# Kernel optimization log

Hardware: AMD Instinct MI355X
Metric: run time of the kernel (lower is better)

The kernel has to match this reference:

```python
import jax, jax.numpy as jnp
import numpy as np

B, L, H = 32, 512, 1024
H2 = H // 2          # split half = 512
D_ATTN = 64
EPS = 1e-5


def setup_inputs() -> dict:
    key = jax.random.key(0)
    ks = jax.random.split(key, 6)
    x = jax.random.normal(ks[0], (B, L, H), dtype=jnp.float32)
    # LayerNorm params (default torch init: weight=1, bias=0)
    ln_gamma = jnp.ones((H2,), jnp.float32)
    ln_beta = jnp.zeros((H2,), jnp.float32)
    # Toeplitz params (module inits w_vector=0, bias=1; use small random w for nontrivial math)
    w_vector = jax.random.normal(ks[1], (2 * L - 1,), jnp.float32) * 0.02
    t_bias = jnp.ones((L,), jnp.float32)
    # TinyAttention: kqv Linear(H2 -> 3*d_attn), proj Linear(d_attn -> H2)
    kqv_w = jax.random.normal(ks[2], (H2, 3 * D_ATTN), jnp.float32) * 0.02
    kqv_b = jnp.zeros((3 * D_ATTN,), jnp.float32)
    proj_w = jax.random.normal(ks[3], (D_ATTN, H2), jnp.float32) * 0.02
    proj_b = jnp.zeros((H2,), jnp.float32)
    return {"x": x, "ln_gamma": ln_gamma, "ln_beta": ln_beta,
            "w_vector": w_vector, "t_bias": t_bias,
            "kqv_w": kqv_w, "kqv_b": kqv_b, "proj_w": proj_w, "proj_b": proj_b}


def _toeplitz(w_vector):
    # Faithful replication of get_toeplitz(): pad, tile, trim, reshape, crop.
    r = w_vector.shape[0] // 2            # = L - 1
    t = jnp.pad(w_vector, (0, L))         # length 3L - 1
    t = jnp.tile(t, L)[:-L]               # length L * (3L - 2)
    t = t.reshape(L, 3 * L - 2)
    return t[:, r:-r]                      # [L, L]


def _tiny_attention(v, kqv_w, kqv_b, proj_w, proj_b):
    kqv = v @ kqv_w + kqv_b                        # [B, L, 3*d_attn]
    k, q, val = jnp.split(kqv, 3, axis=-1)         # chunk order: key, query, value
    scale = 1.0 / jnp.sqrt(jnp.float32(q.shape[-1]))
    scores = jnp.einsum('bqd,bkd->bqk', q, k) * scale
    soft = jax.nn.softmax(scores, axis=-1)
    head = jnp.einsum('bqk,bkd->bqd', soft, val)   # [B, L, d_attn]
    return head @ proj_w + proj_b                  # [B, L, H2]


def reference(x, ln_gamma, ln_beta, w_vector, t_bias, kqv_w, kqv_b, proj_w, proj_b):
    u, v = jnp.split(x, 2, axis=-1)                # each [B, L, H2]
    head = _tiny_attention(v, kqv_w, kqv_b, proj_w, proj_b)
    # LayerNorm over last dim
    mu = jnp.mean(v, axis=-1, keepdims=True)
    var = jnp.mean(jnp.square(v - mu), axis=-1, keepdims=True)
    vn = (v - mu) * jax.lax.rsqrt(var + EPS) * ln_gamma + ln_beta
    # spatial (Toeplitz) mixing: permute -> [B, H2, L], matmul [L, L], bias
    w_t = _toeplitz(w_vector)
    vm = jnp.einsum('blc,lm->bmc', vn, w_t.T).transpose(0, 2, 1)  # keep faithful: vp @ w_t
    vm = jnp.einsum('bcl,lm->bcm', vn.transpose(0, 2, 1), w_t) + t_bias
    v_out = vm.transpose(0, 2, 1) + head           # [B, L, H2]
    return u * v_out
```

## Files before the change

kernel.cpp:

```cpp
#include <hip/hip_runtime.h>
#include <math.h>

#define NB 32
#define LL 512
#define HH 1024
#define H2 512
#define DA 64

typedef unsigned int u32;
typedef unsigned short u16;
typedef __bf16 bf16x8 __attribute__((ext_vector_type(8)));
typedef float f32x4 __attribute__((ext_vector_type(4)));

__device__ __forceinline__ u16 f2bu(float f) {
    u32 u = __builtin_bit_cast(u32, f);
    u = (u + 0x7fff + ((u >> 16) & 1)) >> 16;
    return (u16)u;
}

__device__ __forceinline__ float b2f(u16 u) {
    u32 v = (u32)u << 16;
    return __builtin_bit_cast(float, v);
}

__device__ __forceinline__ void async_cp16(const void* g, void* l) {
    __builtin_amdgcn_global_load_lds(
        (const __attribute__((address_space(1))) u32*)g,
        (__attribute__((address_space(3))) u32*)l, 16, 0, 0);
}

__global__ void prep_kernel(const float* __restrict__ wv,
                            const float* __restrict__ kqvw,
                            const float* __restrict__ projw,
                            u16* __restrict__ wt, u16* __restrict__ kqvwT,
                            u16* __restrict__ projwT) {
    int e = blockIdx.x * 256 + threadIdx.x;
    if (e < 262144) {
        int m = e >> 9, l = e & 511;
        wt[e] = f2bu(wv[511 + m - l]);
    } else if (e < 262144 + 98304) {
        int i = e - 262144;
        int n = i >> 9, k = i & 511;
        kqvwT[i] = f2bu(kqvw[(size_t)k * 192 + n]);
    } else {
        int i = e - 360448;
        int c = i >> 6, d = i & 63;
        projwT[i] = f2bu(projw[(size_t)d * 512 + c]);
    }
}

__global__ __launch_bounds__(256, 2)
void front_kernel(const float* __restrict__ x,
                  const float* __restrict__ gamma, const float* __restrict__ beta,
                  const u16* __restrict__ kqvwT, const float* __restrict__ kqvb,
                  u16* __restrict__ vnT,
                  u16* __restrict__ qb, u16* __restrict__ kb, u16* __restrict__ vT) {
    __shared__ u16 As[32 * 72];
    __shared__ u16 Bs[192 * 64];
    __shared__ u16 T[512 * 34];
    __shared__ float MUs[32], RSs[32];
    int blk = blockIdx.x, t = threadIdx.x;
    int b = blk >> 4, l0 = (blk & 15) * 32;
    int lane = t & 63, wid = t >> 6;
    int l15 = lane & 15, q16 = lane >> 4, q8 = q16 * 8;

#pragma unroll
    for (int s = 0; s < 6; ++s) {
        int ci = t + s * 256;
        int grow = ci >> 3, gcol = ((ci & 7) ^ (grow & 7)) << 3;
        async_cp16(kqvwT + (size_t)grow * 512 + gcol, Bs + ci * 8);
    }

    int r = t >> 3, q = t & 7;
    const float* xr = x + ((size_t)(b * LL + l0 + r)) * HH + H2;
    float s1 = 0.0f, s2 = 0.0f;
#pragma unroll
    for (int i = 0; i < 16; ++i) {
        float4 v = *(const float4*)(xr + q * 64 + i * 4);
        s1 += v.x + v.y + v.z + v.w;
        s2 += v.x * v.x + v.y * v.y + v.z * v.z + v.w * v.w;
        int c = q * 64 + i * 4;
        T[(c + 0) * 34 + r] = f2bu(v.x);
        T[(c + 1) * 34 + r] = f2bu(v.y);
        T[(c + 2) * 34 + r] = f2bu(v.z);
        T[(c + 3) * 34 + r] = f2bu(v.w);
    }
    s1 += __shfl_xor(s1, 1); s2 += __shfl_xor(s2, 1);
    s1 += __shfl_xor(s1, 2); s2 += __shfl_xor(s2, 2);
    s1 += __shfl_xor(s1, 4); s2 += __shfl_xor(s2, 4);
    float mu = s1 * (1.0f / H2);
    float rstd = rsqrtf(s2 * (1.0f / H2) - mu * mu + 1e-5f);
    if ((t & 7) == 0) { MUs[r] = mu; RSs[r] = rstd; }
    __syncthreads();

    {
        int cc = t >> 2, seg = t & 3;
        float m0 = MUs[seg * 8 + 0], r0s = RSs[seg * 8 + 0];
        float m1 = MUs[seg * 8 + 1], r1s = RSs[seg * 8 + 1];
        float m2 = MUs[seg * 8 + 2], r2s = RSs[seg * 8 + 2];
        float m3 = MUs[seg * 8 + 3], r3s = RSs[seg * 8 + 3];
        float m4 = MUs[seg * 8 + 4], r4s = RSs[seg * 8 + 4];
        float m5 = MUs[seg * 8 + 5], r5s = RSs[seg * 8 + 5];
        float m6 = MUs[seg * 8 + 6], r6s = RSs[seg * 8 + 6];
        float m7 = MUs[seg * 8 + 7], r7s = RSs[seg * 8 + 7];
#pragma unroll
        for (int pass = 0; pass < 8; ++pass) {
            int c = pass * 64 + cc;
            float ga = gamma[c], be = beta[c];
            const u16* Tp = T + c * 34 + seg * 8;
            ushort4 t0 = ((const ushort4*)Tp)[0];
            ushort4 t1 = ((const ushort4*)Tp)[1];
            ushort4 o0, o1;
            o0.x = f2bu((b2f(t0.x) - m0) * r0s * ga + be);
            o0.y = f2bu((b2f(t0.y) - m1) * r1s * ga + be);
            o0.z = f2bu((b2f(t0.z) - m2) * r2s * ga + be);
            o0.w = f2bu((b2f(t0.w) - m3) * r3s * ga + be);
            o1.x = f2bu((b2f(t1.x) - m4) * r4s * ga + be);
            o1.y = f2bu((b2f(t1.y) - m5) * r5s * ga + be);
            o1.z = f2bu((b2f(t1.z) - m6) * r6s * ga + be);
            o1.w = f2bu((b2f(t1.w) - m7) * r7s * ga + be);
            u16* dst = vnT + ((size_t)(b * H2 + c)) * LL + l0 + seg * 8;
            ((ushort4*)dst)[0] = o0;
            ((ushort4*)dst)[1] = o1;
        }
    }

    int wm = (wid & 1) * 16, wn = (wid >> 1) * 96;
    f32x4 acc[6] = {};
    for (int k0 = 0; k0 < 512; k0 += 64) {
        if (k0 > 0) {
#pragma unroll
            for (int s = 0; s < 6; ++s) {
                int ci = t + s * 256;
                int grow = ci >> 3, gcol = ((ci & 7) ^ (grow & 7)) << 3;
                async_cp16(kqvwT + (size_t)grow * 512 + k0 + gcol, Bs + ci * 8);
            }
        }
#pragma unroll
        for (int s = 0; s < 2; ++s) {
            int ci = t + s * 256;
            int row = ci >> 4, c4 = (ci & 15) * 4;
            float4 v = *(const float4*)(x + (size_t)(b * LL + l0 + row) * HH + H2 + k0 + c4);
            ushort4 p;
            p.x = f2bu(v.x); p.y = f2bu(v.y); p.z = f2bu(v.z); p.w = f2bu(v.w);
            *(ushort4*)(As + row * 72 + c4) = p;
        }
        __syncthreads();
#pragma unroll
        for (int kk = 0; kk < 2; ++kk) {
            int j0 = kk * 4 + q16;
            bf16x8 a = *(const bf16x8*)(As + (wm + l15) * 72 + kk * 32 + q8);
#pragma unroll
            for (int j = 0; j < 6; ++j) {
                int n = wn + j * 16 + l15;
                bf16x8 bb = *(const bf16x8*)(Bs + (n * 8 + (j0 ^ (n & 7))) * 8);
                acc[j] = __builtin_amdgcn_mfma_f32_16x16x32_bf16(a, bb, acc[j], 0, 0, 0);
            }
        }
        __syncthreads();
    }
    u16* Ts = As;
    int rq = q16 * 4;
#pragma unroll
    for (int rr = 0; rr < 4; ++rr) {
        int mloc = wm + rq + rr;
        size_t mg = (size_t)(b * LL + l0 + mloc);
#pragma unroll
        for (int j = 0; j < 6; ++j) {
            int n = wn + j * 16 + l15;
            u16 hv = f2bu(acc[j][rr] + kqvb[n]);
            if (n < 64)       kb[mg * 64 + n] = hv;
            else if (n < 128) qb[mg * 64 + (n - 64)] = hv;
            else              Ts[(n - 128) * 36 + mloc] = hv;
        }
    }
    __syncthreads();
    int d = t >> 2, lo2 = (t & 3) * 8;
    u16* dst = vT + ((size_t)(b * 64 + d)) * 512 + l0 + lo2;
    const u16* src = Ts + d * 36 + lo2;
    ((ushort4*)dst)[0] = ((const ushort4*)src)[0];
    ((ushort4*)dst)[1] = ((const ushort4*)src)[1];
}

#define VLD 136
__global__ __launch_bounds__(256, 4)
void attn_kernel(const u16* __restrict__ qb, const u16* __restrict__ kb,
                 const u16* __restrict__ vT, u16* __restrict__ head) {
    __shared__ u16 Ps[4 * 16 * VLD];
    __shared__ float Osh[4][16 * 65];
    __shared__ float Msh[4][16], Lsh[4][16];
    int b = blockIdx.y, q0 = blockIdx.x * 16;
    int t = threadIdx.x, lane = t & 63, w = t >> 6;
    int l15 = lane & 15, q16 = lane >> 4, q8 = q16 * 8;
    int kc = w * 128;
    const u16* qg = qb + (size_t)b * LL * DA;
    const u16* kg = kb + (size_t)b * LL * DA;
    const u16* vg = vT + (size_t)b * DA * LL;

    bf16x8 aq[2];
#pragma unroll
    for (int s = 0; s < 2; ++s)
        aq[s] = *(const bf16x8*)(qg + (size_t)(q0 + l15) * DA + s * 32 + q8);

    f32x4 sc[8] = {};
#pragma unroll
    for (int j = 0; j < 8; ++j) {
#pragma unroll
        for (int s = 0; s < 2; ++s) {
            bf16x8 bk = *(const bf16x8*)(kg + (size_t)(kc + j * 16 + l15) * DA + s * 32 + q8);
            sc[j] = __builtin_amdgcn_mfma_f32_16x16x32_bf16(aq[s], bk, sc[j], 0, 0, 0);
        }
    }
    float mx[4], sm[4];
#pragma unroll
    for (int j = 0; j < 8; ++j)
#pragma unroll
        for (int rr = 0; rr < 4; ++rr) sc[j][rr] *= 0.125f;
#pragma unroll
    for (int rr = 0; rr < 4; ++rr) {
        float m0 = sc[0][rr];
#pragma unroll
        for (int j = 1; j < 8; ++j) m0 = fmaxf(m0, sc[j][rr]);
        m0 = fmaxf(m0, __shfl_xor(m0, 1));
        m0 = fmaxf(m0, __shfl_xor(m0, 2));
        m0 = fmaxf(m0, __shfl_xor(m0, 4));
        m0 = fmaxf(m0, __shfl_xor(m0, 8));
        mx[rr] = m0;
    }
#pragma unroll
    for (int j = 0; j < 8; ++j)
#pragma unroll
        for (int rr = 0; rr < 4; ++rr) sc[j][rr] = __expf(sc[j][rr] - mx[rr]);
#pragma unroll
    for (int rr = 0; rr < 4; ++rr) {
        float s0 = sc[0][rr];
#pragma unroll
        for (int j = 1; j < 8; ++j) s0 += sc[j][rr];
        s0 += __shfl_xor(s0, 1);
        s0 += __shfl_xor(s0, 2);
        s0 += __shfl_xor(s0, 4);
        s0 += __shfl_xor(s0, 8);
        sm[rr] = s0;
    }
    u16* Pw = Ps + w * 16 * VLD;
#pragma unroll
    for (int j = 0; j < 8; ++j)
#pragma unroll
        for (int rr = 0; rr < 4; ++rr)
            Pw[(q16 * 4 + rr) * VLD + j * 16 + l15] = f2bu(sc[j][rr]);
    f32x4 o[4] = {};
#pragma unroll
    for (int kt = 0; kt < 4; ++kt) {
        bf16x8 ap = *(const bf16x8*)(Pw + l15 * VLD + kt * 32 + q8);
#pragma unroll
        for (int j = 0; j < 4; ++j) {
            bf16x8 bv = *(const bf16x8*)(vg + (size_t)(j * 16 + l15) * LL + kc + kt * 32 + q8);
            o[j] = __builtin_amdgcn_mfma_f32_16x16x32_bf16(ap, bv, o[j], 0, 0, 0);
        }
    }
#pragma unroll
    for (int j = 0; j < 4; ++j)
#pragma unroll
        for (int rr = 0; rr < 4; ++rr)
            Osh[w][(q16 * 4 + rr) * 65 + j * 16 + l15] = o[j][rr];
    if (l15 == 0) {
#pragma unroll
        for (int rr = 0; rr < 4; ++rr) {
            Msh[w][q16 * 4 + rr] = mx[rr];
            Lsh[w][q16 * 4 + rr] = sm[rr];
        }
    }
    __syncthreads();
    int qq = t >> 4, dg = (t & 15) * 4;
    float m0 = Msh[0][qq], m1 = Msh[1][qq], m2 = Msh[2][qq], m3 = Msh[3][qq];
    float ms = fmaxf(fmaxf(m0, m1), fmaxf(m2, m3));
    float f0 = __expf(m0 - ms), f1 = __expf(m1 - ms), f2 = __expf(m2 - ms), f3 = __expf(m3 - ms);
    float lst = Lsh[0][qq] * f0 + Lsh[1][qq] * f1 + Lsh[2][qq] * f2 + Lsh[3][qq] * f3;
    float inv = 1.0f / lst;
    ushort4 res;
    u16* rp = (u16*)&res;
#pragma unroll
    for (int i = 0; i < 4; ++i) {
        int idx = qq * 65 + dg + i;
        float a = Osh[0][idx] * f0 + Osh[1][idx] * f1 + Osh[2][idx] * f2 + Osh[3][idx] * f3;
        rp[i] = f2bu(a * inv);
    }
    *(ushort4*)(head + (size_t)(b * LL + q0 + qq) * DA + dg) = res;
}

__device__ __forceinline__ void mfma_tile64(const u16* As, const u16* Bs,
                                            f32x4 acc[4][4], int wm, int wn,
                                            int l15, int q16) {
    int s7 = l15 & 7;
#pragma unroll
    for (int kk = 0; kk < 2; ++kk) {
        int j0 = kk * 4 + q16;
        bf16x8 a[4], bv[4];
#pragma unroll
        for (int i = 0; i < 4; ++i) {
            int row = wm + i * 16 + l15;
            a[i] = *(const bf16x8*)(As + (row * 8 + (j0 ^ s7)) * 8);
        }
#pragma unroll
        for (int j = 0; j < 4; ++j) {
            int row = wn + j * 16 + l15;
            bv[j] = *(const bf16x8*)(Bs + (row * 8 + (j0 ^ s7)) * 8);
        }
#pragma unroll
        for (int i = 0; i < 4; ++i)
#pragma unroll
            for (int j = 0; j < 4; ++j)
                acc[i][j] = __builtin_amdgcn_mfma_f32_16x16x32_bf16(a[i], bv[j], acc[i][j], 0, 0, 0);
    }
}

__global__ __launch_bounds__(256, 2)
void mix_kernel(const u16* __restrict__ wt,
                const u16* __restrict__ vnT,
                const u16* __restrict__ headb,
                const u16* __restrict__ projwT,
                const float* __restrict__ x,
                const float* __restrict__ tbias,
                const float* __restrict__ projb,
                float* __restrict__ out) {
    __shared__ u16 As[128 * 64];
    __shared__ u16 Bs[128 * 64];
    int lid = blockIdx.x;
    int p8 = lid & 7, rest = lid >> 3;
    int mi = rest & 3, pair = (rest >> 2) * 8 + p8;
    int b = pair >> 2, m0 = mi * 128, c0 = (pair & 3) * 128;
    int t = threadIdx.x, lane = t & 63, wid = t >> 6;
    int wm = (wid >> 1) * 64, wn = (wid & 1) * 64;
    int l15 = lane & 15, q16 = lane >> 4;
    f32x4 acc[4][4] = {};
    const u16* Ag = wt + (size_t)m0 * 512;
    const u16* Bg = vnT + ((size_t)b * H2 + c0) * 512;
    for (int k0 = 0; k0 < 512; k0 += 64) {
#pragma unroll
        for (int s = 0; s < 4; ++s) {
            int ci = t + s * 256;
            int grow = ci >> 3, gcol = ((ci & 7) ^ (grow & 7)) << 3;
            async_cp16(Ag + (size_t)grow * 512 + k0 + gcol, As + ci * 8);
            async_cp16(Bg + (size_t)grow * 512 + k0 + gcol, Bs + ci * 8);
        }
        __syncthreads();
        mfma_tile64(As, Bs, acc, wm, wn, l15, q16);
        __syncthreads();
    }
    {
        const u16* Hg = headb + ((size_t)b * LL + m0) * DA;
        const u16* Pg = projwT + (size_t)c0 * DA;
#pragma unroll
        for (int s = 0; s < 4; ++s) {
            int ci = t + s * 256;
            int grow = ci >> 3, gcol = ((ci & 7) ^ (grow & 7)) << 3;
            async_cp16(Hg + (size_t)grow * 64 + gcol, As + ci * 8);
            async_cp16(Pg + (size_t)grow * 64 + gcol, Bs + ci * 8);
        }
        __syncthreads();
        mfma_tile64(As, Bs, acc, wm, wn, l15, q16);
        __syncthreads();
    }
    int rq = q16 * 4;
#pragma unroll
    for (int i = 0; i < 4; ++i) {
#pragma unroll
        for (int rr = 0; rr < 4; ++rr) {
            int m = m0 + wm + i * 16 + rq + rr;
            float tb = tbias[m];
            const float* xrow = x + ((size_t)b * LL + m) * HH;
            float* orow = out + ((size_t)b * LL + m) * H2;
#pragma unroll
            for (int j = 0; j < 4; ++j) {
                int c = c0 + wn + j * 16 + l15;
                float val = acc[i][j][rr] + tb + projb[c];
                orow[c] = xrow[c] * val;
            }
        }
    }
}

extern "C" void kernel_launch(void* const* d_in, const int* in_sizes, int n_in,
                              void* d_out, int out_size, void* d_ws, size_t ws_size,
                              hipStream_t stream) {
    (void)in_sizes; (void)n_in; (void)out_size; (void)ws_size;
    const float* x     = (const float*)d_in[0];
    const float* gamma = (const float*)d_in[1];
    const float* beta  = (const float*)d_in[2];
    const float* wv    = (const float*)d_in[3];
    const float* tb    = (const float*)d_in[4];
    const float* kqvw  = (const float*)d_in[5];
    const float* kqvb  = (const float*)d_in[6];
    const float* projw = (const float*)d_in[7];
    const float* projb = (const float*)d_in[8];
    float* out = (float*)d_out;

    u16* vnT_bf  = (u16*)d_ws;
    u16* qb      = vnT_bf + (size_t)NB * LL * H2;
    u16* kb      = qb + (size_t)NB * LL * DA;
    u16* vTb     = kb + (size_t)NB * LL * DA;
    u16* head_bf = vTb + (size_t)NB * LL * DA;
    u16* wt_bf   = head_bf + (size_t)NB * LL * DA;
    u16* kqvwT   = wt_bf + 512 * 512;
    u16* projwT  = kqvwT + 192 * 512;

    prep_kernel <<<1536, 256, 0, stream>>>(wv, kqvw, projw, wt_bf, kqvwT, projwT);
    front_kernel<<<512, 256, 0, stream>>>(x, gamma, beta, kqvwT, kqvb,
                                          vnT_bf, qb, kb, vTb);
    attn_kernel <<<dim3(32, NB), 256, 0, stream>>>(qb, kb, vTb, head_bf);
    mix_kernel  <<<512, 256, 0, stream>>>(wt_bf, vnT_bf, head_bf, projwT,
                                          x, tb, projb, out);
}
```

Measured before the change: 174.4 us.

## Double-buffer LDS staging in front and mix kernels, reuse transposed v tile

The mix kernel now double-buffers its A/B LDS tiles, prefetching the next K-slice (and finally the head/proj tiles) while MFMAs run on the current one, with one barrier per step instead of two. The front kernel's KQV GEMM also double-buffers weight tiles in 32-wide K steps. It builds its A operand from the bf16 transposed v tile already in LDS instead of re-reading x from global memory and converting it. This doubles mix_kernel LDS use to 64KB, which may limit occupancy at two blocks per CU. The A-fragment gather from the transposed tile uses scalar strided LDS reads.

New measurement: 173.5 us. About the same (-0.5%).

```diff
diff --git a/kernel.cpp b/kernel.cpp
--- a/kernel.cpp
+++ b/kernel.cpp
@@ -55,8 +55,7 @@
                   const u16* __restrict__ kqvwT, const float* __restrict__ kqvb,
                   u16* __restrict__ vnT,
                   u16* __restrict__ qb, u16* __restrict__ kb, u16* __restrict__ vT) {
-    __shared__ u16 As[32 * 72];
-    __shared__ u16 Bs[192 * 64];
+    __shared__ u16 Bs[2][192 * 32];
     __shared__ u16 T[512 * 34];
     __shared__ float MUs[32], RSs[32];
     int blk = blockIdx.x, t = threadIdx.x;
@@ -65,10 +64,10 @@
     int l15 = lane & 15, q16 = lane >> 4, q8 = q16 * 8;
 
 #pragma unroll
-    for (int s = 0; s < 6; ++s) {
+    for (int s = 0; s < 3; ++s) {
         int ci = t + s * 256;
-        int grow = ci >> 3, gcol = ((ci & 7) ^ (grow & 7)) << 3;
-        async_cp16(kqvwT + (size_t)grow * 512 + gcol, Bs + ci * 8);
+        int grow = ci >> 2, gcol = ((ci & 3) ^ (grow & 3)) << 3;
+        async_cp16(kqvwT + (size_t)grow * 512 + gcol, &Bs[0][ci * 8]);
     }
 
     int r = t >> 3, q = t & 7;
@@ -126,40 +125,34 @@
     }
 
     int wm = (wid & 1) * 16, wn = (wid >> 1) * 96;
+    int rowA = wm + l15;
     f32x4 acc[6] = {};
-    for (int k0 = 0; k0 < 512; k0 += 64) {
-        if (k0 > 0) {
-#pragma unroll
-            for (int s = 0; s < 6; ++s) {
+    for (int it = 0; it < 16; ++it) {
+        if (it < 15) {
+            int k0n = (it + 1) * 32, bfn = (it + 1) & 1;
+#pragma unroll
+            for (int s = 0; s < 3; ++s) {
                 int ci = t + s * 256;
-                int grow = ci >> 3, gcol = ((ci & 7) ^ (grow & 7)) << 3;
-                async_cp16(kqvwT + (size_t)grow * 512 + k0 + gcol, Bs + ci * 8);
+                int grow = ci >> 2, gcol = ((ci & 3) ^ (grow & 3)) << 3;
+                async_cp16(kqvwT + (size_t)grow * 512 + k0n + gcol, &Bs[bfn][ci * 8]);
             }
         }
-#pragma unroll
-        for (int s = 0; s < 2; ++s) {
-            int ci = t + s * 256;
-            int row = ci >> 4, c4 = (ci & 15) * 4;
-            float4 v = *(const float4*)(x + (size_t)(b * LL + l0 + row) * HH + H2 + k0 + c4);
-            ushort4 p;
-            p.x = f2bu(v.x); p.y = f2bu(v.y); p.z = f2bu(v.z); p.w = f2bu(v.w);
-            *(ushort4*)(As + row * 72 + c4) = p;
+        bf16x8 a;
+        int kb0 = it * 32 + q8;
+#pragma unroll
+        for (int u = 0; u < 8; ++u)
+            a[u] = __builtin_bit_cast(__bf16, T[(kb0 + u) * 34 + rowA]);
+        const u16* Bp = &Bs[it & 1][0];
+#pragma unroll
+        for (int j = 0; j < 6; ++j) {
+            int n = wn + j * 16 + l15;
+            bf16x8 bb = *(const bf16x8*)(Bp + (n * 4 + (q16 ^ (n & 3))) * 8);
+            acc[j] = __builtin_amdgcn_mfma_f32_16x16x32_bf16(a, bb, acc[j], 0, 0, 0);
         }
         __syncthreads();
-#pragma unroll
-        for (int kk = 0; kk < 2; ++kk) {
-            int j0 = kk * 4 + q16;
-            bf16x8 a = *(const bf16x8*)(As + (wm + l15) * 72 + kk * 32 + q8);
-#pragma unroll
-            for (int j = 0; j < 6; ++j) {
-                int n = wn + j * 16 + l15;
-                bf16x8 bb = *(const bf16x8*)(Bs + (n * 8 + (j0 ^ (n & 7))) * 8);
-                acc[j] = __builtin_amdgcn_mfma_f32_16x16x32_bf16(a, bb, acc[j], 0, 0, 0);
-            }
-        }
-        __syncthreads();
-    }
-    u16* Ts = As;
+    }
+
+    u16* Ts = &Bs[0][0];
     int rq = q16 * 4;
 #pragma unroll
     for (int rr = 0; rr < 4; ++rr) {
@@ -314,6 +307,17 @@
     }
 }
 
+__device__ __forceinline__ void stage_pair(const u16* A, const u16* B, int ldk,
+                                           int koff, u16* Ad, u16* Bd, int t) {
+#pragma unroll
+    for (int s = 0; s < 4; ++s) {
+        int ci = t + s * 256;
+        int grow = ci >> 3, gcol = ((ci & 7) ^ (grow & 7)) << 3;
+        async_cp16(A + (size_t)grow * ldk + koff + gcol, Ad + ci * 8);
+        async_cp16(B + (size_t)grow * ldk + koff + gcol, Bd + ci * 8);
+    }
+}
+
 __global__ __launch_bounds__(256, 2)
 void mix_kernel(const u16* __restrict__ wt,
                 const u16* __restrict__ vnT,
@@ -323,8 +327,8 @@
                 const float* __restrict__ tbias,
                 const float* __restrict__ projb,
                 float* __restrict__ out) {
-    __shared__ u16 As[128 * 64];
-    __shared__ u16 Bs[128 * 64];
+    __shared__ u16 As[2][128 * 64];
+    __shared__ u16 Bs[2][128 * 64];
     int lid = blockIdx.x;
     int p8 = lid & 7, rest = lid >> 3;
     int mi = rest & 3, pair = (rest >> 2) * 8 + p8;
@@ -335,32 +339,22 @@
     f32x4 acc[4][4] = {};
     const u16* Ag = wt + (size_t)m0 * 512;
     const u16* Bg = vnT + ((size_t)b * H2 + c0) * 512;
-    for (int k0 = 0; k0 < 512; k0 += 64) {
-#pragma unroll
-        for (int s = 0; s < 4; ++s) {
-            int ci = t + s * 256;
-            int grow = ci >> 3, gcol = ((ci & 7) ^ (grow & 7)) << 3;
-            async_cp16(Ag + (size_t)grow * 512 + k0 + gcol, As + ci * 8);
-            async_cp16(Bg + (size_t)grow * 512 + k0 + gcol, Bs + ci * 8);
-        }
+    const u16* Hg = headb + ((size_t)b * LL + m0) * DA;
+    const u16* Pg = projwT + (size_t)c0 * DA;
+
+    stage_pair(Ag, Bg, 512, 0, As[0], Bs[0], t);
+    __syncthreads();
+
+    for (int it = 0; it < 9; ++it) {
+        int nx = it + 1;
+        if (nx < 8)
+            stage_pair(Ag, Bg, 512, nx * 64, As[nx & 1], Bs[nx & 1], t);
+        else if (nx == 8)
+            stage_pair(Hg, Pg, 64, 0, As[0], Bs[0], t);
+        mfma_tile64(As[it & 1], Bs[it & 1], acc, wm, wn, l15, q16);
         __syncthreads();
-        mfma_tile64(As, Bs, acc, wm, wn, l15, q16);
-        __syncthreads();
-    }
-    {
-        const u16* Hg = headb + ((size_t)b * LL + m0) * DA;
-        const u16* Pg = projwT + (size_t)c0 * DA;
-#pragma unroll
-        for (int s = 0; s < 4; ++s) {
-            int ci = t + s * 256;
-            int grow = ci >> 3, gcol = ((ci & 7) ^ (grow & 7)) << 3;
-            async_cp16(Hg + (size_t)grow * 64 + gcol, As + ci * 8);
-            async_cp16(Pg + (size_t)grow * 64 + gcol, Bs + ci * 8);
-        }
-        __syncthreads();
-        mfma_tile64(As, Bs, acc, wm, wn, l15, q16);
-        __syncthreads();
-    }
+    }
+
     int rq = q16 * 4;
 #pragma unroll
     for (int i = 0; i < 4; ++i) {
```
